# Kernel tuning notes

Measured on AMD Instinct MI355X. Metric: run time of the kernel, lower is better.

Reference implementation:

```python
import jax, jax.numpy as jnp
import numpy as np

D_MODEL = 1024
N_EXPERTS = 8
TOP_K = 2
LN_EPS = 1e-5


def setup_inputs() -> dict:
    key = jax.random.key(0)
    ks = jax.random.split(key, 8)
    B, S, d, E = 2, 2048, D_MODEL, N_EXPERTS
    f = 2 * d
    s_in = 0.02
    return {
        "x": jax.random.normal(ks[0], (B, S, d), jnp.float32),
        "Wg": jax.random.normal(ks[1], (d, E), jnp.float32) * s_in,
        "bg": jnp.zeros((E,), jnp.float32),
        "W1": jax.random.normal(ks[2], (E, d, f), jnp.float32) * s_in,
        "b1": jnp.zeros((E, f), jnp.float32),
        "W2": jax.random.normal(ks[3], (E, f, d), jnp.float32) * s_in,
        "b2": jnp.zeros((E, d), jnp.float32),
        "gamma": jnp.ones((d,), jnp.float32),
        "beta": jnp.zeros((d,), jnp.float32),
    }


def reference(x, Wg, bg, W1, b1, W2, b2, gamma, beta):
    # Gating + top-k routing (softmax over the selected top-k logits only)
    logits = jnp.einsum("bsd,de->bse", x, Wg) + bg            # [B,S,E]
    topk_vals, topk_idx = jax.lax.top_k(logits, TOP_K)         # [B,S,K]
    topk_w = jax.nn.softmax(topk_vals, axis=-1)                # [B,S,K]

    # Expert MLPs evaluated densely for all experts (dropout is identity in eval)
    h = jax.nn.relu(jnp.einsum("bsd,edf->bsef", x, W1) + b1)   # [B,S,E,2d]
    eo = jnp.einsum("bsef,efd->bsed", h, W2) + b2              # [B,S,E,d]

    # Gather the top-k experts' outputs per token and combine with gate weights
    sel = jnp.take_along_axis(eo, topk_idx[..., None], axis=2)  # [B,S,K,d]
    mixed = jnp.sum(sel * topk_w[..., None], axis=2)            # [B,S,d]

    # Residual + LayerNorm
    y = mixed + x
    mu = jnp.mean(y, axis=-1, keepdims=True)
    var = jnp.mean(jnp.square(y - mu), axis=-1, keepdims=True)
    return gamma * (y - mu) * jax.lax.rsqrt(var + LN_EPS) + beta
```

## Files before the change

### kernel.cpp

```cpp
#include <hip/hip_runtime.h>


typedef unsigned short ushort_t;
typedef short short8 __attribute__((ext_vector_type(8)));
typedef float f32x4 __attribute__((ext_vector_type(4)));

#define T_TOKENS 4096
#define DMODEL 1024
#define FFN 2048
#define NEXP 8
#define MAXSLOTS 9216
#define GATE_BLOCKS 1024
#define TOK_PER_BLK 4
#define MAX_MT 12

__device__ __forceinline__ ushort_t f2bf(float f) {
    unsigned u = __float_as_uint(f);
    return (ushort_t)((u + 0x7fffu + ((u >> 16) & 1u)) >> 16);
}
__device__ __forceinline__ float bflo(unsigned packed) {
    return __uint_as_float(packed << 16);
}
__device__ __forceinline__ float bfhi(unsigned packed) {
    return __uint_as_float(packed & 0xffff0000u);
}

__device__ __forceinline__ void gload_lds16(const void* g, void* l) {
    __builtin_amdgcn_global_load_lds(
        (const __attribute__((address_space(1))) unsigned int*)g,
        (__attribute__((address_space(3))) unsigned int*)l,
        16, 0, 0);
}

__global__ __launch_bounds__(256) void gate_kernel(
    const float* __restrict__ x, const float* __restrict__ Wg,
    const float* __restrict__ bg,
    int* __restrict__ top_idx, float* __restrict__ top_w,
    int* __restrict__ blk_hist)
{
    __shared__ int hist[NEXP];
    const int tid = threadIdx.x, lane = tid & 63, w = tid >> 6;
    if (tid < NEXP) hist[tid] = 0;
    __syncthreads();

    const int t = blockIdx.x * TOK_PER_BLK + w;
    const float* xr = x + (size_t)t * DMODEL;
    float acc[8] = {0.f,0.f,0.f,0.f,0.f,0.f,0.f,0.f};
    #pragma unroll
    for (int i = 0; i < 16; i++) {
        float xv = xr[i * 64 + lane];
        const float4* wp = (const float4*)&Wg[(i * 64 + lane) * 8];
        float4 a = wp[0], b = wp[1];
        acc[0] += xv * a.x; acc[1] += xv * a.y;
        acc[2] += xv * a.z; acc[3] += xv * a.w;
        acc[4] += xv * b.x; acc[5] += xv * b.y;
        acc[6] += xv * b.z; acc[7] += xv * b.w;
    }
    #pragma unroll
    for (int off = 32; off > 0; off >>= 1) {
        #pragma unroll
        for (int e = 0; e < 8; e++) acc[e] += __shfl_down(acc[e], off);
    }
    if (lane == 0) {
        float l[8];
        #pragma unroll
        for (int e = 0; e < 8; e++) l[e] = acc[e] + bg[e];
        int i0 = 0; float v0 = l[0];
        #pragma unroll
        for (int e = 1; e < 8; e++) if (l[e] > v0) { v0 = l[e]; i0 = e; }
        int i1 = -1; float v1 = -1e30f;
        #pragma unroll
        for (int e = 0; e < 8; e++) if (e != i0 && l[e] > v1) { v1 = l[e]; i1 = e; }
        float eg = expf(v1 - v0);
        float den = 1.f + eg;
        int p0 = atomicAdd(&hist[i0], 1);
        int p1 = atomicAdd(&hist[i1], 1);
        top_idx[2 * t]     = i0 | (p0 << 4);
        top_idx[2 * t + 1] = i1 | (p1 << 4);
        top_w[2 * t]     = 1.f / den;
        top_w[2 * t + 1] = eg / den;
    }
    __syncthreads();
    if (tid < NEXP) blk_hist[blockIdx.x * NEXP + tid] = hist[tid];
}

__global__ __launch_bounds__(512) void scan_kernel(
    const int* __restrict__ blk_hist, int* __restrict__ blk_base,
    int* __restrict__ offs)
{
    __shared__ int cnt[NEXP];
    const int tid = threadIdx.x, lane = tid & 63, e = tid >> 6;
    int orig[GATE_BLOCKS / 64];
    #pragma unroll
    for (int r = 0; r < GATE_BLOCKS / 64; r++)
        orig[r] = blk_hist[(r * 64 + lane) * NEXP + e];
    int carry = 0;
    #pragma unroll
    for (int r = 0; r < GATE_BLOCKS / 64; r++) {
        int v = orig[r];
        #pragma unroll
        for (int off = 1; off < 64; off <<= 1) {
            int u = __shfl_up(v, off);
            if (lane >= off) v += u;
        }
        blk_base[(r * 64 + lane) * NEXP + e] = carry + v - orig[r];
        carry += __shfl(v, 63);
    }
    if (lane == 0) cnt[e] = carry;
    __syncthreads();
    if (tid == 0) {
        int cum = 0;
        for (int ee = 0; ee < NEXP; ee++) {
            offs[ee] = cum;
            cum += (cnt[ee] + 127) & ~127;
        }
        offs[NEXP] = cum;
    }
}

__global__ __launch_bounds__(256) void scatter_gather_kernel(
    const float* __restrict__ x, const int* __restrict__ top_idx,
    const int* __restrict__ offs, const int* __restrict__ blk_base,
    int* __restrict__ slot_of, ushort_t* __restrict__ Xg)
{
    const int t = blockIdx.x, tid = threadIdx.x;
    __shared__ int slots[2];
    if (tid < 2) {
        int v = top_idx[2 * t + tid];
        int e = v & 15, pos = v >> 4;
        int gb = t / TOK_PER_BLK;
        int slot = offs[e] + blk_base[gb * NEXP + e] + pos;
        slot_of[2 * t + tid] = slot;
        slots[tid] = slot;
    }
    __syncthreads();
    float4 xv = ((const float4*)(x + (size_t)t * DMODEL))[tid];
    uint2 pk;
    pk.x = f2bf(xv.x) | ((unsigned)f2bf(xv.y) << 16);
    pk.y = f2bf(xv.z) | ((unsigned)f2bf(xv.w) << 16);
    ((uint2*)(Xg + (size_t)slots[0] * DMODEL))[tid] = pk;
    ((uint2*)(Xg + (size_t)slots[1] * DMODEL))[tid] = pk;
}

__global__ __launch_bounds__(256) void transpose_kernel(
    const float* __restrict__ W1, const float* __restrict__ W2,
    ushort_t* __restrict__ W1T, ushort_t* __restrict__ W2T)
{
    int b = blockIdx.x;
    const float* s; ushort_t* d; int Rs, Cs, rt, ct;
    if (b < 1024) {
        int e = b >> 7, t = b & 127;
        rt = t >> 4; ct = t & 15;
        s = W1 + (size_t)e * DMODEL * FFN;
        d = W1T + (size_t)e * DMODEL * FFN;
        Rs = DMODEL; Cs = FFN;
    } else {
        b -= 1024;
        int e = b >> 7, t = b & 127;
        rt = t >> 3; ct = t & 7;
        s = W2 + (size_t)e * DMODEL * FFN;
        d = W2T + (size_t)e * DMODEL * FFN;
        Rs = FFN; Cs = DMODEL;
    }
    const int r0 = rt * 128, c0 = ct * 128;
    const int tid = threadIdx.x;

    __shared__ float tile[128][129];

    {
        const int rr = tid >> 5;
        const int cc = (tid & 31) * 4;
        #pragma unroll
        for (int p = 0; p < 16; p++) {
            int r = p * 8 + rr;
            float4 v = *(const float4*)&s[(size_t)(r0 + r) * Cs + c0 + cc];
            tile[r][cc + 0] = v.x;
            tile[r][cc + 1] = v.y;
            tile[r][cc + 2] = v.z;
            tile[r][cc + 3] = v.w;
        }
    }
    __syncthreads();

    {
        const int c  = tid >> 1;
        const int h  = (tid & 1) * 64;
        ushort_t* drow = d + (size_t)(c0 + c) * Rs + r0 + h;
        #pragma unroll
        for (int g = 0; g < 8; g++) {
            uint4 o;
            o.x = (unsigned)f2bf(tile[h + g * 8 + 0][c]) | ((unsigned)f2bf(tile[h + g * 8 + 1][c]) << 16);
            o.y = (unsigned)f2bf(tile[h + g * 8 + 2][c]) | ((unsigned)f2bf(tile[h + g * 8 + 3][c]) << 16);
            o.z = (unsigned)f2bf(tile[h + g * 8 + 4][c]) | ((unsigned)f2bf(tile[h + g * 8 + 5][c]) << 16);
            o.w = (unsigned)f2bf(tile[h + g * 8 + 6][c]) | ((unsigned)f2bf(tile[h + g * 8 + 7][c]) << 16);
            *(uint4*)&drow[g * 8] = o;
        }
    }
}

template <int K, int N, bool RELU>
__global__ __launch_bounds__(256) void expert_gemm(
    const ushort_t* __restrict__ A,
    const ushort_t* __restrict__ Bt,
    const float* __restrict__ bias,
    ushort_t* __restrict__ Cout,
    const int* __restrict__ offs)
{
    const int e  = blockIdx.x;
    const int nt = blockIdx.y;
    const int mt = blockIdx.z;
    const int off_e = offs[e];
    const int Mpad  = offs[e + 1] - off_e;
    if (mt * 128 >= Mpad) return;

    __shared__ __align__(16) ushort_t As[128 * 32];
    __shared__ __align__(16) ushort_t Bs[128 * 32];

    const int tid  = threadIdx.x;
    const int lane = tid & 63;
    const int w    = tid >> 6;
    const int quad = lane >> 4;
    const int r16  = lane & 15;
    const int lrow = lane >> 2;
    const int lk   = (((lane & 3) ^ ((lane >> 3) & 3))) * 8;

    const size_t arow0 = (size_t)(off_e + mt * 128);
    const ushort_t* aS0 = A + (arow0 + (size_t)(2 * w + 0) * 16 + lrow) * K + lk;
    const ushort_t* aS1 = A + (arow0 + (size_t)(2 * w + 1) * 16 + lrow) * K + lk;
    const ushort_t* Bte = Bt + (size_t)e * N * K;
    const ushort_t* bS0 = Bte + ((size_t)(nt * 128 + (2 * w + 0) * 16 + lrow)) * K + lk;
    const ushort_t* bS1 = Bte + ((size_t)(nt * 128 + (2 * w + 1) * 16 + lrow)) * K + lk;
    ushort_t* aD0 = &As[(2 * w + 0) * 512];
    ushort_t* aD1 = &As[(2 * w + 1) * 512];
    ushort_t* bD0 = &Bs[(2 * w + 0) * 512];
    ushort_t* bD1 = &Bs[(2 * w + 1) * 512];

    const int wm = (w >> 1) * 64;
    const int wn = (w & 1) * 64;
    const int sw = ((r16 >> 1) & 3) ^ quad;

    f32x4 acc[4][4];
    #pragma unroll
    for (int i = 0; i < 4; i++)
        #pragma unroll
        for (int j = 0; j < 4; j++)
            acc[i][j] = (f32x4){0.f, 0.f, 0.f, 0.f};

    for (int k0 = 0; k0 < K; k0 += 32) {
        gload_lds16(aS0 + k0, aD0);
        gload_lds16(aS1 + k0, aD1);
        gload_lds16(bS0 + k0, bD0);
        gload_lds16(bS1 + k0, bD1);
        __syncthreads();
        short8 af[4], bfr[4];
        #pragma unroll
        for (int i = 0; i < 4; i++)
            af[i] = *(const short8*)&As[(wm + i * 16 + r16) * 32 + sw * 8];
        #pragma unroll
        for (int j = 0; j < 4; j++)
            bfr[j] = *(const short8*)&Bs[(wn + j * 16 + r16) * 32 + sw * 8];
        #pragma unroll
        for (int i = 0; i < 4; i++)
            #pragma unroll
            for (int j = 0; j < 4; j++)
                acc[i][j] = __builtin_amdgcn_mfma_f32_16x16x32_bf16(
                    af[i], bfr[j], acc[i][j], 0, 0, 0);
        __syncthreads();
    }

    const float* be = bias + (size_t)e * N;
    #pragma unroll
    for (int i = 0; i < 4; i++) {
        #pragma unroll
        for (int j = 0; j < 4; j++) {
            int n = nt * 128 + wn + j * 16 + r16;
            float bv = be[n];
            #pragma unroll
            for (int r = 0; r < 4; r++) {
                int m = mt * 128 + wm + i * 16 + quad * 4 + r;
                float v = acc[i][j][r] + bv;
                if (RELU) v = v > 0.f ? v : 0.f;
                Cout[(size_t)(off_e + m) * N + n] = f2bf(v);
            }
        }
    }
}

__global__ __launch_bounds__(256) void ln_kernel(
    const float* __restrict__ x, const ushort_t* __restrict__ O,
    const int* __restrict__ slot_of, const float* __restrict__ top_w,
    const float* __restrict__ gamma, const float* __restrict__ beta,
    float* __restrict__ out)
{
    int t = blockIdx.x, tid = threadIdx.x;
    int s0 = slot_of[2 * t], s1 = slot_of[2 * t + 1];
    float w0 = top_w[2 * t], w1 = top_w[2 * t + 1];
    float4 xv = ((const float4*)(x + (size_t)t * DMODEL))[tid];
    uint2 a = ((const uint2*)(O + (size_t)s0 * DMODEL))[tid];
    uint2 b = ((const uint2*)(O + (size_t)s1 * DMODEL))[tid];

    float y[4];
    y[0] = xv.x + w0 * bflo(a.x) + w1 * bflo(b.x);
    y[1] = xv.y + w0 * bfhi(a.x) + w1 * bfhi(b.x);
    y[2] = xv.z + w0 * bflo(a.y) + w1 * bflo(b.y);
    y[3] = xv.w + w0 * bfhi(a.y) + w1 * bfhi(b.y);

    float s = y[0] + y[1] + y[2] + y[3];
    float sq = y[0]*y[0] + y[1]*y[1] + y[2]*y[2] + y[3]*y[3];
    __shared__ float red[2][4];
    #pragma unroll
    for (int off = 32; off > 0; off >>= 1) {
        s += __shfl_down(s, off);
        sq += __shfl_down(sq, off);
    }
    int lane = tid & 63, wv = tid >> 6;
    if (lane == 0) { red[0][wv] = s; red[1][wv] = sq; }
    __syncthreads();
    if (tid == 0) {
        float S = red[0][0] + red[0][1] + red[0][2] + red[0][3];
        float SQ = red[1][0] + red[1][1] + red[1][2] + red[1][3];
        float mu = S * (1.f / DMODEL);
        float var = SQ * (1.f / DMODEL) - mu * mu;
        red[0][0] = mu;
        red[1][0] = rsqrtf(var + 1e-5f);
    }
    __syncthreads();
    float mu = red[0][0], inv = red[1][0];
    float4 gv = ((const float4*)gamma)[tid];
    float4 bv = ((const float4*)beta)[tid];
    float4 ov;
    ov.x = gv.x * (y[0] - mu) * inv + bv.x;
    ov.y = gv.y * (y[1] - mu) * inv + bv.y;
    ov.z = gv.z * (y[2] - mu) * inv + bv.z;
    ov.w = gv.w * (y[3] - mu) * inv + bv.w;
    ((float4*)(out + (size_t)t * DMODEL))[tid] = ov;
}

extern "C" void kernel_launch(void* const* d_in, const int* in_sizes, int n_in,
                              void* d_out, int out_size, void* d_ws, size_t ws_size,
                              hipStream_t stream)
{
    const float* x     = (const float*)d_in[0];
    const float* Wg    = (const float*)d_in[1];
    const float* bg    = (const float*)d_in[2];
    const float* W1    = (const float*)d_in[3];
    const float* b1    = (const float*)d_in[4];
    const float* W2    = (const float*)d_in[5];
    const float* b2    = (const float*)d_in[6];
    const float* gamma = (const float*)d_in[7];
    const float* beta  = (const float*)d_in[8];
    float* out = (float*)d_out;

    char* ws = (char*)d_ws;
    size_t o = 0;
    auto alloc = [&](size_t bytes) {
        size_t r = o;
        o = (o + bytes + 255) & ~(size_t)255;
        return r;
    };
    size_t o_offs    = alloc((NEXP + 1) * 4);
    size_t o_topidx  = alloc((size_t)T_TOKENS * 2 * 4);
    size_t o_topw    = alloc((size_t)T_TOKENS * 2 * 4);
    size_t o_slotof  = alloc((size_t)T_TOKENS * 2 * 4);
    size_t o_bhist   = alloc((size_t)GATE_BLOCKS * NEXP * 4);
    size_t o_bbase   = alloc((size_t)GATE_BLOCKS * NEXP * 4);
    size_t o_w1t     = alloc((size_t)NEXP * DMODEL * FFN * 2);
    size_t o_w2t     = alloc((size_t)NEXP * DMODEL * FFN * 2);
    size_t o_xg      = alloc((size_t)MAXSLOTS * DMODEL * 2);
    size_t o_h       = alloc((size_t)MAXSLOTS * FFN * 2);
    size_t o_obuf    = alloc((size_t)MAXSLOTS * DMODEL * 2);
    (void)ws_size; (void)in_sizes; (void)n_in; (void)out_size;

    int*      offs     = (int*)(ws + o_offs);
    int*      top_idx  = (int*)(ws + o_topidx);
    float*    top_w    = (float*)(ws + o_topw);
    int*      slot_of  = (int*)(ws + o_slotof);
    int*      blk_hist = (int*)(ws + o_bhist);
    int*      blk_base = (int*)(ws + o_bbase);
    ushort_t* W1T      = (ushort_t*)(ws + o_w1t);
    ushort_t* W2T      = (ushort_t*)(ws + o_w2t);
    ushort_t* Xg       = (ushort_t*)(ws + o_xg);
    ushort_t* H        = (ushort_t*)(ws + o_h);
    ushort_t* Obuf     = (ushort_t*)(ws + o_obuf);

    gate_kernel<<<GATE_BLOCKS, 256, 0, stream>>>(x, Wg, bg, top_idx, top_w, blk_hist);
    transpose_kernel<<<2048, 256, 0, stream>>>(W1, W2, W1T, W2T);
    scan_kernel<<<1, 512, 0, stream>>>(blk_hist, blk_base, offs);
    scatter_gather_kernel<<<T_TOKENS, 256, 0, stream>>>(x, top_idx, offs, blk_base, slot_of, Xg);
    expert_gemm<DMODEL, FFN, true>
        <<<dim3(NEXP, FFN / 128, MAX_MT), 256, 0, stream>>>(Xg, W1T, b1, H, offs);
    expert_gemm<FFN, DMODEL, false>
        <<<dim3(NEXP, DMODEL / 128, MAX_MT), 256, 0, stream>>>(H, W2T, b2, Obuf, offs);
    ln_kernel<<<T_TOKENS, 256, 0, stream>>>(x, Obuf, slot_of, top_w, gamma, beta, out);
}
```

Before: 322.5 us.

## Store transposed expert weights in K-chunked blocked layout for contiguous B tile loads

The weight-conversion kernel now writes W1/W2 as bf16 in a blocked layout of 32-wide K chunks, each storing N rows of 32 contiguous elements, and it converts to bf16 before staging through a smaller LDS tile. The expert GEMM reads its B operand from this layout, so each K-step's B tile is one contiguous region instead of rows strided by K. This aims to improve DRAM/L2 locality for the weight stream and to cut LDS footprint and conversion work in the transpose. The transpose's LDS reads of 16-bit values may now hit bank conflicts, and the layout is specific to the 32-wide K step.

```diff
diff --git a/kernel.cpp b/kernel.cpp
--- a/kernel.cpp
+++ b/kernel.cpp
@@ -147,53 +147,50 @@
     ushort_t* __restrict__ W1T, ushort_t* __restrict__ W2T)
 {
     int b = blockIdx.x;
-    const float* s; ushort_t* d; int Rs, Cs, rt, ct;
+    const float* s; ushort_t* d; int N, kc, ns;
     if (b < 1024) {
-        int e = b >> 7, t = b & 127;
-        rt = t >> 4; ct = t & 15;
+        int e = b >> 7, idx = b & 127;
+        kc = idx >> 2; ns = idx & 3;
         s = W1 + (size_t)e * DMODEL * FFN;
         d = W1T + (size_t)e * DMODEL * FFN;
-        Rs = DMODEL; Cs = FFN;
+        N = FFN;
     } else {
         b -= 1024;
-        int e = b >> 7, t = b & 127;
-        rt = t >> 3; ct = t & 7;
+        int e = b >> 7, idx = b & 127;
+        kc = idx >> 1; ns = idx & 1;
         s = W2 + (size_t)e * DMODEL * FFN;
         d = W2T + (size_t)e * DMODEL * FFN;
-        Rs = FFN; Cs = DMODEL;
-    }
-    const int r0 = rt * 128, c0 = ct * 128;
+        N = DMODEL;
+    }
+    const int k0 = kc * 32, n0 = ns * 512;
     const int tid = threadIdx.x;
 
-    __shared__ float tile[128][129];
+    __shared__ __align__(16) ushort_t lt[32][516];
+
+    #pragma unroll
+    for (int i = 0; i < 16; i++) {
+        int k = i * 2 + (tid >> 7);
+        int n = (tid & 127) * 4;
+        float4 v = *(const float4*)&s[(size_t)(k0 + k) * N + n0 + n];
+        uint2 pk;
+        pk.x = (unsigned)f2bf(v.x) | ((unsigned)f2bf(v.y) << 16);
+        pk.y = (unsigned)f2bf(v.z) | ((unsigned)f2bf(v.w) << 16);
+        *(uint2*)&lt[k][n] = pk;
+    }
+    __syncthreads();
 
     {
-        const int rr = tid >> 5;
-        const int cc = (tid & 31) * 4;
-        #pragma unroll
-        for (int p = 0; p < 16; p++) {
-            int r = p * 8 + rr;
-            float4 v = *(const float4*)&s[(size_t)(r0 + r) * Cs + c0 + cc];
-            tile[r][cc + 0] = v.x;
-            tile[r][cc + 1] = v.y;
-            tile[r][cc + 2] = v.z;
-            tile[r][cc + 3] = v.w;
-        }
-    }
-    __syncthreads();
-
-    {
-        const int c  = tid >> 1;
-        const int h  = (tid & 1) * 64;
-        ushort_t* drow = d + (size_t)(c0 + c) * Rs + r0 + h;
-        #pragma unroll
-        for (int g = 0; g < 8; g++) {
+        const int sub = tid & 3;
+        const int nl0 = tid >> 2;
+        #pragma unroll
+        for (int it = 0; it < 8; it++) {
+            int n = nl0 + it * 64;
             uint4 o;
-            o.x = (unsigned)f2bf(tile[h + g * 8 + 0][c]) | ((unsigned)f2bf(tile[h + g * 8 + 1][c]) << 16);
-            o.y = (unsigned)f2bf(tile[h + g * 8 + 2][c]) | ((unsigned)f2bf(tile[h + g * 8 + 3][c]) << 16);
-            o.z = (unsigned)f2bf(tile[h + g * 8 + 4][c]) | ((unsigned)f2bf(tile[h + g * 8 + 5][c]) << 16);
-            o.w = (unsigned)f2bf(tile[h + g * 8 + 6][c]) | ((unsigned)f2bf(tile[h + g * 8 + 7][c]) << 16);
-            *(uint4*)&drow[g * 8] = o;
+            o.x = (unsigned)lt[sub * 8 + 0][n] | ((unsigned)lt[sub * 8 + 1][n] << 16);
+            o.y = (unsigned)lt[sub * 8 + 2][n] | ((unsigned)lt[sub * 8 + 3][n] << 16);
+            o.z = (unsigned)lt[sub * 8 + 4][n] | ((unsigned)lt[sub * 8 + 5][n] << 16);
+            o.w = (unsigned)lt[sub * 8 + 6][n] | ((unsigned)lt[sub * 8 + 7][n] << 16);
+            *(uint4*)&d[((size_t)kc * N + n0 + n) * 32 + sub * 8] = o;
         }
     }
 }
@@ -228,8 +225,8 @@
     const ushort_t* aS0 = A + (arow0 + (size_t)(2 * w + 0) * 16 + lrow) * K + lk;
     const ushort_t* aS1 = A + (arow0 + (size_t)(2 * w + 1) * 16 + lrow) * K + lk;
     const ushort_t* Bte = Bt + (size_t)e * N * K;
-    const ushort_t* bS0 = Bte + ((size_t)(nt * 128 + (2 * w + 0) * 16 + lrow)) * K + lk;
-    const ushort_t* bS1 = Bte + ((size_t)(nt * 128 + (2 * w + 1) * 16 + lrow)) * K + lk;
+    const ushort_t* bS0 = Bte + (size_t)(nt * 128 + (2 * w + 0) * 16 + lrow) * 32 + lk;
+    const ushort_t* bS1 = Bte + (size_t)(nt * 128 + (2 * w + 1) * 16 + lrow) * 32 + lk;
     ushort_t* aD0 = &As[(2 * w + 0) * 512];
     ushort_t* aD1 = &As[(2 * w + 1) * 512];
     ushort_t* bD0 = &Bs[(2 * w + 0) * 512];
@@ -249,8 +246,8 @@
     for (int k0 = 0; k0 < K; k0 += 32) {
         gload_lds16(aS0 + k0, aD0);
         gload_lds16(aS1 + k0, aD1);
-        gload_lds16(bS0 + k0, bD0);
-        gload_lds16(bS1 + k0, bD1);
+        gload_lds16(bS0 + (size_t)k0 * N, bD0);
+        gload_lds16(bS1 + (size_t)k0 * N, bD1);
         __syncthreads();
         short8 af[4], bfr[4];
         #pragma unroll
```

Measured after the change: 319.9 us. Within noise of the previous version (-0.8%).
